# Kernel tuning notes

Hardware: AMD Instinct MI355X
Metric: run time of the kernel (lower is better)

Reference implementation:

```python
import jax, jax.numpy as jnp
import numpy as np

N = 200000
C = 384
G = 383            # number of unique target ids (0..G-1 all present w.h.p.)
M = G + 1          # object_num = len(unique) + 1; must equal C for the original broadcast
EPS = 1e-5


def setup_inputs() -> dict:
    key = jax.random.key(0)
    k1, k2 = jax.random.split(key)
    pred_id = jax.random.normal(k1, (N, C), dtype=jnp.float32)
    target_id = jax.random.randint(k2, (N,), 0, G)
    return {"pred_id": pred_id, "target_id": target_id}


def reference(pred_id, target_id):
    seg = target_id  # ids are 0..G-1 and all present -> sorted unique == arange(G)
    dt = pred_id.dtype
    ones = jnp.ones((N,), dtype=dt)
    n_rows = jax.ops.segment_sum(ones, seg, num_segments=G)                 # [G] group sizes
    row_sum = jax.ops.segment_sum(pred_id.sum(axis=1), seg, num_segments=G)  # [G]
    cnt = n_rows * C                                                        # elements per group
    mean = row_sum / cnt                                                    # scalar mean per group
    centered = pred_id - mean[seg][:, None]
    ss = jax.ops.segment_sum((centered * centered).sum(axis=1), seg, num_segments=G)
    # torch .std() is unbiased over all n_i*C elements; 0 if group has a single row
    std = jnp.where(n_rows > 1, jnp.sqrt(ss / jnp.maximum(cnt - 1.0, 1.0)), 0.0)

    # pad the extra (always-zero) object slot -> object_proto/object_std have M rows
    proto = jnp.concatenate([mean, jnp.zeros((1,), dt)])   # [M]; each row of object_proto is constant
    stdv = jnp.concatenate([std, jnp.zeros((1,), dt)])     # [M]

    diff = proto[None, :] - proto[:, None]                 # [M,M] V_dist[x,a,:] is constant over C
    norm = jnp.abs(diff) * jnp.sqrt(jnp.asarray(C, dt))    # ||V_dist||_2 over C channels
    d = jax.lax.stop_gradient(diff / (norm + EPS))         # detached unit direction, [M,M]

    # object_std_i[x,a,b] = |std[a] * d[x,a]|; object_std_j[x,a,b] = |std[b] * d[x,a]|
    si = jnp.abs(stdv[None, :, None] * d[:, :, None])      # [M,M,M]
    sj = jnp.abs(stdv[None, None, :] * d[:, :, None])      # [M,M,M]
    s = si + sj
    V = s / (norm[None, :, :] + s + EPS)                   # V_dist_norm broadcast as [1,M,M]
    mask = jnp.triu(jnp.ones((M, M), dtype=bool), k=1)     # triu(diagonal=1) on last two dims
    V = jnp.where(mask[None, :, :], V, jnp.zeros((), dt))
    return V.mean()
```

## Files before the change

### kernel.cpp

```cpp
#include <hip/hip_runtime.h>
#include <math.h>

#define NROWS 200000
#define C 384
#define G 383
#define M 384
#define EPS 1e-5f
#define SQRTC 19.595917942265423f

#define NBLK1 1024
#define THR1 512
#define NWAVES ((NBLK1 * THR1) / 64)
#define NBLK4 576

#define WS_PART  0
#define WS_S2    (WS_PART + NBLK1 * 1152)
#define WS_PROTO (WS_S2 + 8 * 1152)
#define WS_STD   (WS_PROTO + 384)
#define WS_P3    (WS_STD + 384)

__global__ __launch_bounds__(THR1) void stats_kernel(const float4* __restrict__ pred4,
                                                     const int* __restrict__ tgt,
                                                     float* __restrict__ ws,
                                                     int n_rows) {
    __shared__ float lc[384], ls[384], lq[384];
    const int tid = threadIdx.x;
    for (int i = tid; i < 384; i += THR1) { lc[i] = 0.f; ls[i] = 0.f; lq[i] = 0.f; }
    __syncthreads();

    const int lane = tid & 63;
    const int wv   = (blockIdx.x * THR1 + tid) >> 6;

    for (int row = wv; row < n_rows; row += NWAVES) {
        const float4* rp = pred4 + (size_t)row * 96;
        const int seg = tgt[row];
        float4 v0 = rp[lane];
        float s = (v0.x + v0.y) + (v0.z + v0.w);
        float q = fmaf(v0.x, v0.x, fmaf(v0.y, v0.y, fmaf(v0.z, v0.z, v0.w * v0.w)));
        if (lane < 32) {
            float4 v1 = rp[64 + lane];
            s += (v1.x + v1.y) + (v1.z + v1.w);
            q += fmaf(v1.x, v1.x, fmaf(v1.y, v1.y, fmaf(v1.z, v1.z, v1.w * v1.w)));
        }
#pragma unroll
        for (int off = 32; off > 0; off >>= 1) {
            s += __shfl_down(s, off);
            q += __shfl_down(q, off);
        }
        if (lane == 0) {
            atomicAdd(&lc[seg], 1.0f);
            atomicAdd(&ls[seg], s);
            atomicAdd(&lq[seg], q);
        }
    }
    __syncthreads();

    float* dst = ws + (size_t)blockIdx.x * 1152;
    for (int i = tid; i < 384; i += THR1) {
        dst[i]       = lc[i];
        dst[384 + i] = ls[i];
        dst[768 + i] = lq[i];
    }
}

__global__ void reduce_kernel(float* __restrict__ ws) {
    const int t   = blockIdx.x * blockDim.x + threadIdx.x;
    const int j   = t % 1152;
    const int sub = t / 1152;
    float acc = 0.f;
#pragma unroll 8
    for (int b = sub; b < NBLK1; b += 8)
        acc += ws[WS_PART + (size_t)b * 1152 + j];
    ws[WS_S2 + sub * 1152 + j] = acc;
}

__global__ void finalize_kernel(float* __restrict__ ws) {
    const int g = threadIdx.x;
    float cnt_r = 0.f, sum = 0.f, ss = 0.f;
#pragma unroll
    for (int sub = 0; sub < 8; ++sub) {
        const float* s2 = ws + WS_S2 + sub * 1152;
        cnt_r += s2[g];
        sum   += s2[384 + g];
        ss    += s2[768 + g];
    }
    float mean = 0.f, sd = 0.f;
    if (g < G && cnt_r > 0.5f) {
        float cnt = cnt_r * (float)C;
        mean = sum / cnt;
        if (cnt_r > 1.5f) {
            float cs    = ss - cnt * mean * mean;
            float denom = fmaxf(cnt - 1.0f, 1.0f);
            sd = sqrtf(fmaxf(cs / denom, 0.f));
        }
    }
    ws[WS_PROTO + g] = mean;
    ws[WS_STD + g]   = sd;
}

__global__ void triple_sum_kernel(const float* __restrict__ ws,
                                  float* __restrict__ part3) {
    __shared__ float sp[M];
    __shared__ float sst[M];
    __shared__ float wsum[4];
    const int tid = threadIdx.x;

    for (int i = tid; i < M; i += blockDim.x) {
        sp[i]  = ws[WS_PROTO + i];
        sst[i] = ws[WS_STD + i];
    }
    __syncthreads();

    const int idx = blockIdx.x * blockDim.x + tid;
    float partial = 0.f;
    {
        const int x = idx / M;
        const int a = idx - x * M;
        const float pa = sp[a];
        const float u  = fabsf(pa - sp[x]);
        const float t  = u / (u * SQRTC + EPS);
        if (t > 0.f) {
            const float sa = sst[a];
#pragma unroll 4
            for (int b = a + 1; b < M; ++b) {
                float nab = fabsf(sp[b] - pa) * SQRTC;
                float s   = t * (sa + sst[b]);
                partial += s * __builtin_amdgcn_rcpf(nab + s + EPS);
            }
        }
    }

#pragma unroll
    for (int off = 32; off > 0; off >>= 1)
        partial += __shfl_down(partial, off);
    if ((tid & 63) == 0) wsum[tid >> 6] = partial;
    __syncthreads();
    if (tid == 0)
        part3[blockIdx.x] = wsum[0] + wsum[1] + wsum[2] + wsum[3];
}

__global__ void write_out_kernel(const float* __restrict__ part3,
                                 float* __restrict__ out) {
    __shared__ float wsum[9];
    const int tid = threadIdx.x;
    float v = part3[tid];
#pragma unroll
    for (int off = 32; off > 0; off >>= 1)
        v += __shfl_down(v, off);
    if ((tid & 63) == 0) wsum[tid >> 6] = v;
    __syncthreads();
    if (tid == 0) {
        float acc = 0.f;
#pragma unroll
        for (int w = 0; w < 9; ++w) acc += wsum[w];
        out[0] = acc / ((float)M * (float)M * (float)M);
    }
}

extern "C" void kernel_launch(void* const* d_in, const int* in_sizes, int n_in,
                              void* d_out, int out_size, void* d_ws, size_t ws_size,
                              hipStream_t stream) {
    const float4* pred4 = (const float4*)d_in[0];
    const int*    tgt   = (const int*)d_in[1];
    float* ws  = (float*)d_ws;
    float* out = (float*)d_out;
    const int n_rows = in_sizes[1];

    stats_kernel<<<NBLK1, THR1, 0, stream>>>(pred4, tgt, ws, n_rows);
    reduce_kernel<<<36, 256, 0, stream>>>(ws);
    finalize_kernel<<<1, 384, 0, stream>>>(ws);
    triple_sum_kernel<<<NBLK4, 256, 0, stream>>>(ws, ws + WS_P3);
    write_out_kernel<<<1, 576, 0, stream>>>(ws + WS_P3, out);
}
```

Baseline: 434.7 us.

## Fuse reduce/finalize and triple-sum/write-out via last-block atomic counters

After: 431.1 us (median of 2 runs). About the same (-0.8%).

```diff
diff --git a/kernel.cpp b/kernel.cpp
--- a/kernel.cpp
+++ b/kernel.cpp
@@ -11,6 +11,7 @@
 #define NBLK1 1024
 #define THR1 512
 #define NWAVES ((NBLK1 * THR1) / 64)
+#define NBLK2 24
 #define NBLK4 576
 
 #define WS_PART  0
@@ -18,6 +19,7 @@
 #define WS_PROTO (WS_S2 + 8 * 1152)
 #define WS_STD   (WS_PROTO + 384)
 #define WS_P3    (WS_STD + 384)
+#define WS_CTR   (WS_P3 + NBLK4)
 
 __global__ __launch_bounds__(THR1) void stats_kernel(const float4* __restrict__ pred4,
                                                      const int* __restrict__ tgt,
@@ -25,6 +27,11 @@
                                                      int n_rows) {
     __shared__ float lc[384], ls[384], lq[384];
     const int tid = threadIdx.x;
+    if (blockIdx.x == 0 && tid == 0) {
+        unsigned int* ctr = (unsigned int*)(ws + WS_CTR);
+        ctr[0] = 0u;
+        ctr[1] = 0u;
+    }
     for (int i = tid; i < 384; i += THR1) { lc[i] = 0.f; ls[i] = 0.f; lq[i] = 0.f; }
     __syncthreads();
 
@@ -63,8 +70,9 @@
     }
 }
 
-__global__ void reduce_kernel(float* __restrict__ ws) {
-    const int t   = blockIdx.x * blockDim.x + threadIdx.x;
+__global__ __launch_bounds__(384) void reduce_finalize_kernel(float* __restrict__ ws) {
+    __shared__ int is_last;
+    const int t   = blockIdx.x * 384 + threadIdx.x;
     const int j   = t % 1152;
     const int sub = t / 1152;
     float acc = 0.f;
@@ -72,14 +80,22 @@
     for (int b = sub; b < NBLK1; b += 8)
         acc += ws[WS_PART + (size_t)b * 1152 + j];
     ws[WS_S2 + sub * 1152 + j] = acc;
-}
 
-__global__ void finalize_kernel(float* __restrict__ ws) {
+    __threadfence();
+    __syncthreads();
+    if (threadIdx.x == 0) {
+        unsigned int* ctr = (unsigned int*)(ws + WS_CTR);
+        is_last = (atomicAdd(&ctr[0], 1u) == NBLK2 - 1);
+    }
+    __syncthreads();
+    if (!is_last) return;
+    __threadfence();
+
     const int g = threadIdx.x;
     float cnt_r = 0.f, sum = 0.f, ss = 0.f;
 #pragma unroll
-    for (int sub = 0; sub < 8; ++sub) {
-        const float* s2 = ws + WS_S2 + sub * 1152;
+    for (int sub2 = 0; sub2 < 8; ++sub2) {
+        const float* s2 = ws + WS_S2 + sub2 * 1152;
         cnt_r += s2[g];
         sum   += s2[384 + g];
         ss    += s2[768 + g];
@@ -98,35 +114,35 @@
     ws[WS_STD + g]   = sd;
 }
 
-__global__ void triple_sum_kernel(const float* __restrict__ ws,
-                                  float* __restrict__ part3) {
+__global__ __launch_bounds__(256) void triple_write_kernel(float* __restrict__ ws,
+                                                           float* __restrict__ out) {
     __shared__ float sp[M];
     __shared__ float sst[M];
     __shared__ float wsum[4];
+    __shared__ int is_last;
     const int tid = threadIdx.x;
 
-    for (int i = tid; i < M; i += blockDim.x) {
+    for (int i = tid; i < M; i += 256) {
         sp[i]  = ws[WS_PROTO + i];
         sst[i] = ws[WS_STD + i];
     }
     __syncthreads();
 
-    const int idx = blockIdx.x * blockDim.x + tid;
+    const int idx = blockIdx.x * 256 + tid;
+    const int a   = idx / M;
+    const int x   = idx - a * M;
     float partial = 0.f;
     {
-        const int x = idx / M;
-        const int a = idx - x * M;
         const float pa = sp[a];
+        const float sa = sst[a];
         const float u  = fabsf(pa - sp[x]);
-        const float t  = u / (u * SQRTC + EPS);
-        if (t > 0.f) {
-            const float sa = sst[a];
+        const float tt = u / (u * SQRTC + EPS);
+        const float tsa = tt * sa;
 #pragma unroll 4
-            for (int b = a + 1; b < M; ++b) {
-                float nab = fabsf(sp[b] - pa) * SQRTC;
-                float s   = t * (sa + sst[b]);
-                partial += s * __builtin_amdgcn_rcpf(nab + s + EPS);
-            }
+        for (int b = a + 1; b < M; ++b) {
+            float nab = fabsf(sp[b] - pa) * SQRTC;
+            float s   = fmaf(tt, sst[b], tsa);
+            partial += s * __builtin_amdgcn_rcpf(nab + s + EPS);
         }
     }
 
@@ -135,24 +151,26 @@
         partial += __shfl_down(partial, off);
     if ((tid & 63) == 0) wsum[tid >> 6] = partial;
     __syncthreads();
-    if (tid == 0)
-        part3[blockIdx.x] = wsum[0] + wsum[1] + wsum[2] + wsum[3];
-}
+    if (tid == 0) {
+        ws[WS_P3 + blockIdx.x] = wsum[0] + wsum[1] + wsum[2] + wsum[3];
+        __threadfence();
+        unsigned int* ctr = (unsigned int*)(ws + WS_CTR);
+        is_last = (atomicAdd(&ctr[1], 1u) == NBLK4 - 1);
+    }
+    __syncthreads();
+    if (!is_last) return;
+    __threadfence();
 
-__global__ void write_out_kernel(const float* __restrict__ part3,
-                                 float* __restrict__ out) {
-    __shared__ float wsum[9];
-    const int tid = threadIdx.x;
-    float v = part3[tid];
+    float v = ws[WS_P3 + tid] + ws[WS_P3 + 256 + tid];
+    if (tid < 64) v += ws[WS_P3 + 512 + tid];
 #pragma unroll
     for (int off = 32; off > 0; off >>= 1)
         v += __shfl_down(v, off);
-    if ((tid & 63) == 0) wsum[tid >> 6] = v;
+    __shared__ float fsum[4];
+    if ((tid & 63) == 0) fsum[tid >> 6] = v;
     __syncthreads();
     if (tid == 0) {
-        float acc = 0.f;
-#pragma unroll
-        for (int w = 0; w < 9; ++w) acc += wsum[w];
+        float acc = (fsum[0] + fsum[1]) + (fsum[2] + fsum[3]);
         out[0] = acc / ((float)M * (float)M * (float)M);
     }
 }
@@ -167,8 +185,6 @@
     const int n_rows = in_sizes[1];
 
     stats_kernel<<<NBLK1, THR1, 0, stream>>>(pred4, tgt, ws, n_rows);
-    reduce_kernel<<<36, 256, 0, stream>>>(ws);
-    finalize_kernel<<<1, 384, 0, stream>>>(ws);
-    triple_sum_kernel<<<NBLK4, 256, 0, stream>>>(ws, ws + WS_P3);
-    write_out_kernel<<<1, 576, 0, stream>>>(ws + WS_P3, out);
+    reduce_finalize_kernel<<<NBLK2, 384, 0, stream>>>(ws);
+    triple_write_kernel<<<NBLK4, 256, 0, stream>>>(ws, out);
 }
```
